# Performance work log

Hardware: AMD Instinct MI355X
Metric: run time of the kernel (lower is better)

The kernel has to match this reference:

```python
import jax, jax.numpy as jnp
import numpy as np

B = 65536       # number of segments (molecules/graphs) = max(batch_indices[0]) + 1
N = 1048576     # nodes per eye
IN_NF, R_OUT, C_OUT = 64, 128, 128
BRAIN_IN, BRAIN_H, BRAIN_OUT = 256, 256, 128


def setup_inputs() -> dict:
    key = jax.random.key(0)
    ks = jax.random.split(key, 16)
    f = jax.random.normal
    s_in = 1.0 / np.sqrt(IN_NF)
    s_r = 1.0 / np.sqrt(R_OUT)
    s_b = 1.0 / np.sqrt(BRAIN_IN)
    s_h = 1.0 / np.sqrt(BRAIN_H)
    return {
        "x0": f(ks[0], (N, IN_NF), jnp.float32),
        "x1": f(ks[1], (N, IN_NF), jnp.float32),
        "idx0": jax.random.randint(ks[2], (N,), 0, B, dtype=jnp.int32),
        "idx1": jax.random.randint(ks[3], (N,), 0, B, dtype=jnp.int32),
        "Wr0": f(ks[4], (IN_NF, R_OUT), jnp.float32) * s_in,
        "br0": jnp.zeros((R_OUT,), jnp.float32),
        "Wc0": f(ks[5], (R_OUT, C_OUT), jnp.float32) * s_r,
        "bc0": jnp.zeros((C_OUT,), jnp.float32),
        "Wr1": f(ks[6], (IN_NF, R_OUT), jnp.float32) * s_in,
        "br1": jnp.zeros((R_OUT,), jnp.float32),
        "Wc1": f(ks[7], (R_OUT, C_OUT), jnp.float32) * s_r,
        "bc1": jnp.zeros((C_OUT,), jnp.float32),
        "Wb1": f(ks[8], (BRAIN_IN, BRAIN_H), jnp.float32) * s_b,
        "bb1": jnp.zeros((BRAIN_H,), jnp.float32),
        "Wb2": f(ks[9], (BRAIN_H, BRAIN_OUT), jnp.float32) * s_h,
        "bb2": jnp.zeros((BRAIN_OUT,), jnp.float32),
    }


def _eye(x, idx, Wr, br, Wc, bc):
    # linear + relu per node: [N, r_out]
    h = jax.nn.relu(x @ Wr + br)
    # scatter-mean over segments -> [B, r_out]; empty segments get 0 (matches
    # torch_scatter mean and the original zero-padding up to maxlen)
    s = jax.ops.segment_sum(h, idx, num_segments=B)
    cnt = jax.ops.segment_sum(jnp.ones((h.shape[0],), h.dtype), idx, num_segments=B)
    mean = s / jnp.maximum(cnt, 1.0)[:, None]
    # per-graph linear + relu -> [B, c_out]
    return jax.nn.relu(mean @ Wc + bc)


def reference(x0, x1, idx0, idx1, Wr0, br0, Wc0, bc0, Wr1, br1, Wc1, bc1, Wb1, bb1, Wb2, bb2):
    e0 = _eye(x0, idx0, Wr0, br0, Wc0, bc0)   # [B, 128]
    e1 = _eye(x1, idx1, Wr1, br1, Wc1, bc1)   # [B, 128]
    z = jnp.concatenate([e0, e1], axis=1)      # [B, 256]
    h = jax.nn.relu(z @ Wb1 + bb1)             # [B, 256]
    return h @ Wb2 + bb2                       # [B, 128]
```

## Files before the change

### kernel.cpp

```cpp
#include <hip/hip_runtime.h>
#include <hip/hip_bf16.h>

#define B_SEG 65536
#define N_NODES 1048576

typedef _Float16 f16;
typedef __attribute__((ext_vector_type(8))) _Float16 f16x8;
typedef __attribute__((ext_vector_type(2))) __fp16 fp16x2;
typedef __attribute__((ext_vector_type(4))) float f32x4;

union F16x8 { f16x8 v; fp16x2 h2[4]; };

__global__ __launch_bounds__(256) void histo_part(const int* __restrict__ idx0,
        const int* __restrict__ idx1, int* __restrict__ cnt0, int* __restrict__ cnt1) {
    int part  = blockIdx.x & 7;
    int chunk = blockIdx.x >> 3;
    int base  = chunk * (N_NODES / 256);
    for (int i = base + threadIdx.x; i < base + N_NODES / 256; i += 256) {
        int s0 = idx0[i];
        if ((s0 >> 13) == part) atomicAdd(&cnt0[s0], 1);
        int s1 = idx1[i];
        if ((s1 >> 13) == part) atomicAdd(&cnt1[s1], 1);
    }
}

__global__ __launch_bounds__(256) void scan1(const int* __restrict__ cnt, int* __restrict__ bsum) {
    int b = blockIdx.x, t = threadIdx.x;
    int4 v = ((const int4*)cnt)[b * 256 + t];
    int s = v.x + v.y + v.z + v.w;
    for (int d = 1; d < 64; d <<= 1) s += __shfl_xor(s, d);
    __shared__ int ws4[4];
    if ((t & 63) == 0) ws4[t >> 6] = s;
    __syncthreads();
    if (t == 0) bsum[b] = ws4[0] + ws4[1] + ws4[2] + ws4[3];
}

__global__ __launch_bounds__(128) void scan2(int* __restrict__ bsum) {
    int t = threadIdx.x, lane = t & 63;
    int v = bsum[t];
    int s = v;
    for (int d = 1; d < 64; d <<= 1) { int u = __shfl_up(s, d); if (lane >= d) s += u; }
    bsum[t] = s - v;
}

__global__ __launch_bounds__(256) void scan3(int* __restrict__ cnt, const int* __restrict__ bsum,
                                             int* __restrict__ off0, int* __restrict__ off1) {
    int b = blockIdx.x, t = threadIdx.x;
    int4 v = ((const int4*)cnt)[b * 256 + t];
    int local = v.x + v.y + v.z + v.w;
    int lane = t & 63, w = t >> 6;
    int s = local;
    for (int d = 1; d < 64; d <<= 1) { int u = __shfl_up(s, d); if (lane >= d) s += u; }
    __shared__ int wsum[4];
    if (lane == 63) wsum[w] = s;
    __syncthreads();
    int carry = bsum[b];
    for (int i = 0; i < w; ++i) carry += wsum[i];
    int ex = carry + s - local;
    int* off = (b < 64) ? off0 : off1;
    int gi = (b & 63) * 1024 + t * 4;
    off[gi] = ex; ex += v.x; off[gi + 1] = ex; ex += v.y; off[gi + 2] = ex; ex += v.z; off[gi + 3] = ex;
    int4 z; z.x = 0; z.y = 0; z.z = 0; z.w = 0;
    ((int4*)cnt)[b * 256 + t] = z;
    if (b == 0 && t == 0) { off0[B_SEG] = N_NODES; off1[B_SEG] = N_NODES; }
}

__global__ __launch_bounds__(256) void fill_part(const int* __restrict__ idx0,
        const int* __restrict__ idx1, const int* __restrict__ off0, const int* __restrict__ off1,
        int* __restrict__ cur0, int* __restrict__ cur1,
        int* __restrict__ ord0, int* __restrict__ ord1) {
    int part  = blockIdx.x & 7;
    int chunk = blockIdx.x >> 3;
    int base  = chunk * (N_NODES / 256);
    for (int i = base + threadIdx.x; i < base + N_NODES / 256; i += 256) {
        int s0 = idx0[i];
        if ((s0 >> 13) == part) { int p = atomicAdd(&cur0[s0], 1); ord0[off0[s0] + p] = i; }
        int s1 = idx1[i];
        if ((s1 >> 13) == part) { int p = atomicAdd(&cur1[s1], 1); ord1[off1[s1] + p] = i; }
    }
}

__global__ __launch_bounds__(256) void prep_weights(
        const float* __restrict__ Wc0, const float* __restrict__ Wc1,
        const float* __restrict__ Wb1, const float* __restrict__ Wb2,
        f16* __restrict__ T0, f16* __restrict__ T1, f16* __restrict__ T2, f16* __restrict__ T3) {
    int b = blockIdx.x, t = threadIdx.x;
    if (b < 64)        { int i = b * 256 + t;         T0[i] = (f16)Wc0[(i & 127) * 128 + (i >> 7)]; }
    else if (b < 128)  { int i = (b - 64) * 256 + t;  T1[i] = (f16)Wc1[(i & 127) * 128 + (i >> 7)]; }
    else if (b < 384)  { int i = (b - 128) * 256 + t; T2[i] = (f16)Wb1[(i & 255) * 256 + (i >> 8)]; }
    else               { int i = (b - 384) * 256 + t; T3[i] = (f16)Wb2[(i & 255) * 128 + (i >> 8)]; }
}

#define SEGS_PER_WAVE 8
__global__ __launch_bounds__(256, 3) void eye_means_mfma(
        const float* __restrict__ x, const float* __restrict__ Wr,
        const float* __restrict__ br, const int* __restrict__ off,
        const int* __restrict__ ord, f16* __restrict__ means) {
    int lane = threadIdx.x & 63;
    int wid  = blockIdx.x * 4 + (threadIdx.x >> 6);
    int c  = lane & 15;
    int kq = lane >> 4;

    f16x8 bfr[8][2];
    float rbias[8];
    #pragma unroll
    for (int g = 0; g < 8; ++g) {
        #pragma unroll
        for (int h = 0; h < 2; ++h)
            #pragma unroll
            for (int j = 0; j < 8; ++j)
                bfr[g][h][j] = (f16)Wr[(size_t)(h * 32 + kq * 8 + j) * 128 + g * 16 + c];
        rbias[g] = br[g * 16 + c];
    }

    int s_begin = wid * SEGS_PER_WAVE;
    int offv  = off[s_begin + ((lane <= 8) ? lane : 8)];
    int base0 = __shfl(offv, 0);
    int nxtv  = __shfl(offv, (lane < 8) ? (lane + 1) : 8);
    int szl   = nxtv - offv;

    int ov0 = ord[base0 + lane];
    int ov1 = ord[base0 + 64 + lane];
    int ov2 = ord[base0 + 128 + lane];

    auto node_at = [&](int off_rel, int sz, int r) -> int {
        int e  = off_rel + r;
        int e6 = e & 63;
        int n0 = __shfl(ov0, e6);
        int n1 = __shfl(ov1, e6);
        int n2 = __shfl(ov2, e6);
        int n  = (e < 64) ? n0 : (e < 128) ? n1 : n2;
        if (e >= 192) n = ord[base0 + e];
        return (r < sz) ? n : 0;
    };

    auto loadx = [&](int node, float4& v0, float4& v1, float4& v2, float4& v3) {
        const float* xp = &x[(size_t)node * 64 + kq * 8];
        v0 = *(const float4*)(xp);      v1 = *(const float4*)(xp + 4);
        v2 = *(const float4*)(xp + 32); v3 = *(const float4*)(xp + 36);
    };

    float sum[8];
    #pragma unroll
    for (int g = 0; g < 8; ++g) sum[g] = 0.f;

    float4 ca, cb, cc, cd;
    {
        int sz0 = __shfl(szl, 0);
        loadx(node_at(0, sz0, c), ca, cb, cc, cd);
    }

    #pragma unroll
    for (int s = 0; s < SEGS_PER_WAVE; ++s) {
        int off_rel   = __shfl(offv, s) - base0;
        int sz        = __shfl(szl, s);
        int nb        = (sz + 15) >> 4;
        int off_rel_n = (s < SEGS_PER_WAVE - 1) ? (__shfl(offv, s + 1) - base0) : 0;
        int sz_n      = (s < SEGS_PER_WAVE - 1) ? __shfl(szl, s + 1) : 0;
        size_t mb     = (size_t)(s_begin + s) * 128;

        if (nb == 0) {
            means[mb + (2 * kq + 0) * 16 + c] = (f16)0.f;
            means[mb + (2 * kq + 1) * 16 + c] = (f16)0.f;
            loadx(node_at(off_rel_n, sz_n, c), ca, cb, cc, cd);
            continue;
        }

        for (int b = 0; b < nb; ++b) {
            int nn = (b + 1 < nb) ? node_at(off_rel, sz, (b + 1) * 16 + c)
                                  : node_at(off_rel_n, sz_n, c);
            float4 pa, pb, pc, pd;
            loadx(nn, pa, pb, pc, pd);

            f16x8 A0 = {}, A1 = {};
            if (b * 16 + c < sz) {
                F16x8 u0, u1;
                u0.h2[0] = __builtin_amdgcn_cvt_pkrtz(ca.x, ca.y);
                u0.h2[1] = __builtin_amdgcn_cvt_pkrtz(ca.z, ca.w);
                u0.h2[2] = __builtin_amdgcn_cvt_pkrtz(cb.x, cb.y);
                u0.h2[3] = __builtin_amdgcn_cvt_pkrtz(cb.z, cb.w);
                u1.h2[0] = __builtin_amdgcn_cvt_pkrtz(cc.x, cc.y);
                u1.h2[1] = __builtin_amdgcn_cvt_pkrtz(cc.z, cc.w);
                u1.h2[2] = __builtin_amdgcn_cvt_pkrtz(cd.x, cd.y);
                u1.h2[3] = __builtin_amdgcn_cvt_pkrtz(cd.z, cd.w);
                A0 = u0.v; A1 = u1.v;
            }
            #pragma unroll
            for (int g = 0; g < 8; ++g) {
                f32x4 acc = {0.f, 0.f, 0.f, 0.f};
                acc = __builtin_amdgcn_mfma_f32_16x16x32_f16(A0, bfr[g][0], acc, 0, 0, 0);
                acc = __builtin_amdgcn_mfma_f32_16x16x32_f16(A1, bfr[g][1], acc, 0, 0, 0);
                #pragma unroll
                for (int r = 0; r < 4; ++r)
                    sum[g] += fmaxf(acc[r] + rbias[g], 0.f);
            }
            ca = pa; cb = pb; cc = pc; cd = pd;
        }

        float padc = (float)(nb * 16 - sz);
        float inv  = 1.f / (float)sz;
        #pragma unroll
        for (int g = 0; g < 8; ++g) {
            float v = sum[g];
            v += __shfl_xor(v, 16);
            v += __shfl_xor(v, 32);
            v -= padc * fmaxf(rbias[g], 0.f);
            sum[g] = v * inv;
        }
        means[mb + (2 * kq + 0) * 16 + c] = (f16)sum[2 * kq + 0];
        means[mb + (2 * kq + 1) * 16 + c] = (f16)sum[2 * kq + 1];
        #pragma unroll
        for (int g = 0; g < 8; ++g) sum[g] = 0.f;
    }
}

template<int K, int RELU, int OUT16>
__global__ __launch_bounds__(256) void gemm16(
        const f16* __restrict__ A, const f16* __restrict__ BT,
        const float* __restrict__ bias, void* __restrict__ Cv, int ldc) {
    int lane = threadIdx.x & 63;
    int w = threadIdx.x >> 6;
    int c = lane & 15, kq = lane >> 4;
    int m0 = blockIdx.x * 128 + w * 32;
    int n0 = blockIdx.y * 128;

    f32x4 acc[2][8] = {};
    const f16* arow0 = A + (size_t)(m0 + c) * K + kq * 8;
    const f16* arow1 = arow0 + (size_t)16 * K;
    const f16* brow  = BT + (size_t)(n0 + c) * K + kq * 8;

    #pragma unroll 2
    for (int k0 = 0; k0 < K; k0 += 32) {
        f16x8 a0 = *(const f16x8*)(arow0 + k0);
        f16x8 a1 = *(const f16x8*)(arow1 + k0);
        #pragma unroll
        for (int g = 0; g < 8; ++g) {
            f16x8 bf = *(const f16x8*)(brow + (size_t)g * 16 * K + k0);
            acc[0][g] = __builtin_amdgcn_mfma_f32_16x16x32_f16(a0, bf, acc[0][g], 0, 0, 0);
            acc[1][g] = __builtin_amdgcn_mfma_f32_16x16x32_f16(a1, bf, acc[1][g], 0, 0, 0);
        }
    }

    #pragma unroll
    for (int g = 0; g < 8; ++g) {
        float bv = bias[n0 + g * 16 + c];
        #pragma unroll
        for (int ms = 0; ms < 2; ++ms) {
            #pragma unroll
            for (int r = 0; r < 4; ++r) {
                float v = acc[ms][g][r] + bv;
                if (RELU) v = fmaxf(v, 0.f);
                size_t ci = (size_t)(m0 + ms * 16 + kq * 4 + r) * ldc + n0 + g * 16 + c;
                if (OUT16) ((f16*)Cv)[ci] = (f16)v;
                else       ((float*)Cv)[ci] = v;
            }
        }
    }
}

extern "C" void kernel_launch(void* const* d_in, const int* in_sizes, int n_in,
                              void* d_out, int out_size, void* d_ws, size_t ws_size,
                              hipStream_t stream) {
    const float* x0  = (const float*)d_in[0];
    const float* x1  = (const float*)d_in[1];
    const int*   idx0 = (const int*)d_in[2];
    const int*   idx1 = (const int*)d_in[3];
    const float* Wr0 = (const float*)d_in[4];
    const float* br0 = (const float*)d_in[5];
    const float* Wc0 = (const float*)d_in[6];
    const float* bc0 = (const float*)d_in[7];
    const float* Wr1 = (const float*)d_in[8];
    const float* br1 = (const float*)d_in[9];
    const float* Wc1 = (const float*)d_in[10];
    const float* bc1 = (const float*)d_in[11];
    const float* Wb1 = (const float*)d_in[12];
    const float* bb1 = (const float*)d_in[13];
    const float* Wb2 = (const float*)d_in[14];
    const float* bb2 = (const float*)d_in[15];
    float* out = (float*)d_out;

    char* w = (char*)d_ws;
    auto alloc = [&](size_t bytes) { void* p = (void*)w; w += (bytes + 255) & ~(size_t)255; return p; };
    int* cnt0 = (int*)alloc((size_t)B_SEG * 4);
    int* cnt1 = (int*)alloc((size_t)B_SEG * 4);
    int* off0 = (int*)alloc((size_t)(B_SEG + 1) * 4);
    int* off1 = (int*)alloc((size_t)(B_SEG + 1) * 4);
    int* ord0 = (int*)alloc((size_t)(N_NODES + 256) * 4);
    int* ord1 = (int*)alloc((size_t)(N_NODES + 256) * 4);
    int* bsum = (int*)alloc(128 * 4);
    f16* means0 = (f16*)alloc((size_t)B_SEG * 128 * 2);
    f16* means1 = (f16*)alloc((size_t)B_SEG * 128 * 2);
    f16* z      = (f16*)alloc((size_t)B_SEG * 256 * 2);
    f16* hb     = (f16*)alloc((size_t)B_SEG * 256 * 2);
    f16* T0     = (f16*)alloc((size_t)128 * 128 * 2);
    f16* T1     = (f16*)alloc((size_t)128 * 128 * 2);
    f16* T2     = (f16*)alloc((size_t)256 * 256 * 2);
    f16* T3     = (f16*)alloc((size_t)128 * 256 * 2);

    (void)hipMemsetAsync(cnt0, 0, 2 * (size_t)B_SEG * sizeof(int), stream);
    histo_part<<<2048, 256, 0, stream>>>(idx0, idx1, cnt0, cnt1);
    scan1<<<128, 256, 0, stream>>>(cnt0, bsum);
    scan2<<<1, 128, 0, stream>>>(bsum);
    scan3<<<128, 256, 0, stream>>>(cnt0, bsum, off0, off1);
    fill_part<<<2048, 256, 0, stream>>>(idx0, idx1, off0, off1, cnt0, cnt1, ord0, ord1);
    prep_weights<<<512, 256, 0, stream>>>(Wc0, Wc1, Wb1, Wb2, T0, T1, T2, T3);

    eye_means_mfma<<<2048, 256, 0, stream>>>(x0, Wr0, br0, off0, ord0, means0);
    eye_means_mfma<<<2048, 256, 0, stream>>>(x1, Wr1, br1, off1, ord1, means1);

    gemm16<128, 1, 1><<<dim3(512, 1), 256, 0, stream>>>(means0, T0, bc0, z,       256);
    gemm16<128, 1, 1><<<dim3(512, 1), 256, 0, stream>>>(means1, T1, bc1, z + 128, 256);
    gemm16<256, 1, 1><<<dim3(512, 2), 256, 0, stream>>>(z,  T2, bb1, hb,  256);
    gemm16<256, 0, 0><<<dim3(512, 1), 256, 0, stream>>>(hb, T3, bb2, out, 128);
}
```

Baseline: 454.2 us.

## Fuse brain MLP GEMM chain into one kernel and batch both eyes

The four separate GEMM launches (two eye projections, brain layer 1, brain layer 2) become a single kernel. Each wave keeps its 32-row intermediate activations in LDS instead of writing the z and hb buffers to global memory and reading them back. The two eye_means launches are merged into one grid, with blockIdx.y choosing the eye. This removes the intermediate HBM traffic and launch gaps. In exchange it adds about 67KB of LDS per block, which may limit occupancy, and the layer-1 output with 256 columns is now computed entirely by one wave.

After: 510.2 us. +12.3%, slower.

```diff
diff --git a/kernel.cpp b/kernel.cpp
--- a/kernel.cpp
+++ b/kernel.cpp
@@ -10,6 +10,8 @@
 typedef __attribute__((ext_vector_type(4))) float f32x4;
 
 union F16x8 { f16x8 v; fp16x2 h2[4]; };
+
+#define MFMA16(a, b, acc) __builtin_amdgcn_mfma_f32_16x16x32_f16((a), (b), (acc), 0, 0, 0)
 
 __global__ __launch_bounds__(256) void histo_part(const int* __restrict__ idx0,
         const int* __restrict__ idx1, int* __restrict__ cnt0, int* __restrict__ cnt1) {
@@ -93,9 +95,14 @@
 
 #define SEGS_PER_WAVE 8
 __global__ __launch_bounds__(256, 3) void eye_means_mfma(
-        const float* __restrict__ x, const float* __restrict__ Wr,
-        const float* __restrict__ br, const int* __restrict__ off,
-        const int* __restrict__ ord, f16* __restrict__ means) {
+        const float* __restrict__ xA, const float* __restrict__ WrA, const float* __restrict__ brA,
+        const int* __restrict__ offA, const int* __restrict__ ordA, f16* __restrict__ meansA,
+        const float* __restrict__ xB, const float* __restrict__ WrB, const float* __restrict__ brB,
+        const int* __restrict__ offB, const int* __restrict__ ordB, f16* __restrict__ meansB) {
+    const float *x, *Wr, *br; const int *off, *ord; f16* means;
+    if (blockIdx.y == 0) { x = xA; Wr = WrA; br = brA; off = offA; ord = ordA; means = meansA; }
+    else                 { x = xB; Wr = WrB; br = brB; off = offB; ord = ordB; means = meansB; }
+
     int lane = threadIdx.x & 63;
     int wid  = blockIdx.x * 4 + (threadIdx.x >> 6);
     int c  = lane & 15;
@@ -188,8 +195,8 @@
             #pragma unroll
             for (int g = 0; g < 8; ++g) {
                 f32x4 acc = {0.f, 0.f, 0.f, 0.f};
-                acc = __builtin_amdgcn_mfma_f32_16x16x32_f16(A0, bfr[g][0], acc, 0, 0, 0);
-                acc = __builtin_amdgcn_mfma_f32_16x16x32_f16(A1, bfr[g][1], acc, 0, 0, 0);
+                acc = MFMA16(A0, bfr[g][0], acc);
+                acc = MFMA16(A1, bfr[g][1], acc);
                 #pragma unroll
                 for (int r = 0; r < 4; ++r)
                     sum[g] += fmaxf(acc[r] + rbias[g], 0.f);
@@ -214,47 +221,92 @@
     }
 }
 
-template<int K, int RELU, int OUT16>
-__global__ __launch_bounds__(256) void gemm16(
-        const f16* __restrict__ A, const f16* __restrict__ BT,
-        const float* __restrict__ bias, void* __restrict__ Cv, int ldc) {
+__global__ __launch_bounds__(256) void brain_fused(
+        const f16* __restrict__ means0, const f16* __restrict__ means1,
+        const f16* __restrict__ T0, const f16* __restrict__ T1,
+        const f16* __restrict__ T2, const f16* __restrict__ T3,
+        const float* __restrict__ bc0, const float* __restrict__ bc1,
+        const float* __restrict__ bb1, const float* __restrict__ bb2,
+        float* __restrict__ out) {
+    __shared__ f16 Esl[4][32][264];
     int lane = threadIdx.x & 63;
     int w = threadIdx.x >> 6;
     int c = lane & 15, kq = lane >> 4;
     int m0 = blockIdx.x * 128 + w * 32;
-    int n0 = blockIdx.y * 128;
-
-    f32x4 acc[2][8] = {};
-    const f16* arow0 = A + (size_t)(m0 + c) * K + kq * 8;
-    const f16* arow1 = arow0 + (size_t)16 * K;
-    const f16* brow  = BT + (size_t)(n0 + c) * K + kq * 8;
-
-    #pragma unroll 2
-    for (int k0 = 0; k0 < K; k0 += 32) {
-        f16x8 a0 = *(const f16x8*)(arow0 + k0);
-        f16x8 a1 = *(const f16x8*)(arow1 + k0);
+    auto S = Esl[w];
+
+    #pragma unroll
+    for (int e = 0; e < 2; ++e) {
+        const f16* M  = e ? means1 : means0;
+        const f16* W  = e ? T1 : T0;
+        const float* bc = e ? bc1 : bc0;
+        f32x4 acc[2][8] = {};
+        #pragma unroll
+        for (int k0 = 0; k0 < 128; k0 += 32) {
+            f16x8 a0 = *(const f16x8*)&M[(size_t)(m0 + c) * 128 + kq * 8 + k0];
+            f16x8 a1 = *(const f16x8*)&M[(size_t)(m0 + 16 + c) * 128 + kq * 8 + k0];
+            #pragma unroll
+            for (int g = 0; g < 8; ++g) {
+                f16x8 bf = *(const f16x8*)&W[(size_t)(g * 16 + c) * 128 + kq * 8 + k0];
+                acc[0][g] = MFMA16(a0, bf, acc[0][g]);
+                acc[1][g] = MFMA16(a1, bf, acc[1][g]);
+            }
+        }
         #pragma unroll
         for (int g = 0; g < 8; ++g) {
-            f16x8 bf = *(const f16x8*)(brow + (size_t)g * 16 * K + k0);
-            acc[0][g] = __builtin_amdgcn_mfma_f32_16x16x32_f16(a0, bf, acc[0][g], 0, 0, 0);
-            acc[1][g] = __builtin_amdgcn_mfma_f32_16x16x32_f16(a1, bf, acc[1][g], 0, 0, 0);
-        }
-    }
-
+            float bv = bc[g * 16 + c];
+            #pragma unroll
+            for (int ms = 0; ms < 2; ++ms)
+                #pragma unroll
+                for (int r = 0; r < 4; ++r)
+                    S[ms * 16 + kq * 4 + r][e * 128 + g * 16 + c] =
+                        (f16)fmaxf(acc[ms][g][r] + bv, 0.f);
+        }
+    }
+
+    f32x4 acc2[2][16] = {};
+    #pragma unroll
+    for (int k0 = 0; k0 < 256; k0 += 32) {
+        f16x8 a0 = *(const f16x8*)&S[c][k0 + kq * 8];
+        f16x8 a1 = *(const f16x8*)&S[16 + c][k0 + kq * 8];
+        #pragma unroll
+        for (int g = 0; g < 16; ++g) {
+            f16x8 bf = *(const f16x8*)&T2[(size_t)(g * 16 + c) * 256 + kq * 8 + k0];
+            acc2[0][g] = MFMA16(a0, bf, acc2[0][g]);
+            acc2[1][g] = MFMA16(a1, bf, acc2[1][g]);
+        }
+    }
+    #pragma unroll
+    for (int g = 0; g < 16; ++g) {
+        float bv = bb1[g * 16 + c];
+        #pragma unroll
+        for (int ms = 0; ms < 2; ++ms)
+            #pragma unroll
+            for (int r = 0; r < 4; ++r)
+                S[ms * 16 + kq * 4 + r][g * 16 + c] = (f16)fmaxf(acc2[ms][g][r] + bv, 0.f);
+    }
+
+    f32x4 acc3[2][8] = {};
+    #pragma unroll
+    for (int k0 = 0; k0 < 256; k0 += 32) {
+        f16x8 a0 = *(const f16x8*)&S[c][k0 + kq * 8];
+        f16x8 a1 = *(const f16x8*)&S[16 + c][k0 + kq * 8];
+        #pragma unroll
+        for (int g = 0; g < 8; ++g) {
+            f16x8 bf = *(const f16x8*)&T3[(size_t)(g * 16 + c) * 256 + kq * 8 + k0];
+            acc3[0][g] = MFMA16(a0, bf, acc3[0][g]);
+            acc3[1][g] = MFMA16(a1, bf, acc3[1][g]);
+        }
+    }
     #pragma unroll
     for (int g = 0; g < 8; ++g) {
-        float bv = bias[n0 + g * 16 + c];
-        #pragma unroll
-        for (int ms = 0; ms < 2; ++ms) {
-            #pragma unroll
-            for (int r = 0; r < 4; ++r) {
-                float v = acc[ms][g][r] + bv;
-                if (RELU) v = fmaxf(v, 0.f);
-                size_t ci = (size_t)(m0 + ms * 16 + kq * 4 + r) * ldc + n0 + g * 16 + c;
-                if (OUT16) ((f16*)Cv)[ci] = (f16)v;
-                else       ((float*)Cv)[ci] = v;
-            }
-        }
+        float bv = bb2[g * 16 + c];
+        #pragma unroll
+        for (int ms = 0; ms < 2; ++ms)
+            #pragma unroll
+            for (int r = 0; r < 4; ++r)
+                out[(size_t)(m0 + ms * 16 + kq * 4 + r) * 128 + g * 16 + c] =
+                    acc3[ms][g][r] + bv;
     }
 }
 
@@ -290,8 +342,6 @@
     int* bsum = (int*)alloc(128 * 4);
     f16* means0 = (f16*)alloc((size_t)B_SEG * 128 * 2);
     f16* means1 = (f16*)alloc((size_t)B_SEG * 128 * 2);
-    f16* z      = (f16*)alloc((size_t)B_SEG * 256 * 2);
-    f16* hb     = (f16*)alloc((size_t)B_SEG * 256 * 2);
     f16* T0     = (f16*)alloc((size_t)128 * 128 * 2);
     f16* T1     = (f16*)alloc((size_t)128 * 128 * 2);
     f16* T2     = (f16*)alloc((size_t)256 * 256 * 2);
@@ -305,11 +355,10 @@
     fill_part<<<2048, 256, 0, stream>>>(idx0, idx1, off0, off1, cnt0, cnt1, ord0, ord1);
     prep_weights<<<512, 256, 0, stream>>>(Wc0, Wc1, Wb1, Wb2, T0, T1, T2, T3);
 
-    eye_means_mfma<<<2048, 256, 0, stream>>>(x0, Wr0, br0, off0, ord0, means0);
-    eye_means_mfma<<<2048, 256, 0, stream>>>(x1, Wr1, br1, off1, ord1, means1);
-
-    gemm16<128, 1, 1><<<dim3(512, 1), 256, 0, stream>>>(means0, T0, bc0, z,       256);
-    gemm16<128, 1, 1><<<dim3(512, 1), 256, 0, stream>>>(means1, T1, bc1, z + 128, 256);
-    gemm16<256, 1, 1><<<dim3(512, 2), 256, 0, stream>>>(z,  T2, bb1, hb,  256);
-    gemm16<256, 0, 0><<<dim3(512, 1), 256, 0, stream>>>(hb, T3, bb2, out, 128);
-}
+    eye_means_mfma<<<dim3(2048, 2), 256, 0, stream>>>(
+        x0, Wr0, br0, off0, ord0, means0,
+        x1, Wr1, br1, off1, ord1, means1);
+
+    brain_fused<<<512, 256, 0, stream>>>(means0, means1, T0, T1, T2, T3,
+                                         bc0, bc1, bb1, bb2, out);
+}
```
